# Kernel optimization log

Hardware: AMD Instinct MI355X
Metric: run time of the kernel (lower is better)

## Reference

```python
import jax, jax.numpy as jnp
import numpy as np

B, F_SP, F_DN, VOCAB, EMB = 16384, 26, 13, 100000, 16


def setup_inputs() -> dict:
    key = jax.random.key(0)
    ks = jax.random.split(key, 9)
    sparse_inputs = jax.random.randint(ks[0], (B, F_SP), 0, VOCAB, dtype=jnp.int32)
    dense_inputs = jax.random.normal(ks[1], (B, F_DN), dtype=jnp.float32)
    s = 0.02
    return {
        "sparse_inputs": sparse_inputs,
        "dense_inputs": dense_inputs,
        "linear_dense_W": jax.random.normal(ks[2], (F_DN, 1), jnp.float32) * s,
        "linear_dense_b": jnp.zeros((1,), jnp.float32),
        "linear_emb": jax.random.normal(ks[3], (F_SP, VOCAB, 1), jnp.float32) * s,  # per-feature 1-d linear embeddings
        "fm_emb": jax.random.normal(ks[4], (F_SP, VOCAB, EMB), jnp.float32) * s,    # per-feature FM embeddings
        "finish_W": jax.random.normal(ks[5], (1, 1), jnp.float32) * s,
        "finish_b": jnp.zeros((1,), jnp.float32),
        "like_W": jax.random.normal(ks[6], (1, 1), jnp.float32) * s,
        "like_b": jnp.zeros((1,), jnp.float32),
    }


def reference(sparse_inputs, dense_inputs, linear_dense_W, linear_dense_b,
              linear_emb, fm_emb, finish_W, finish_b, like_W, like_b):
    feat_idx = jnp.arange(F_SP)[None, :]  # [1, F]

    # first-order: dense linear + sum of 1-d sparse embeddings
    lin_dense = dense_inputs @ linear_dense_W + linear_dense_b          # [B, 1]
    lin_sparse = linear_emb[feat_idx, sparse_inputs]                    # [B, F, 1]
    first_order = lin_dense + jnp.sum(lin_sparse, axis=1)               # [B, 1]

    # second-order FM: 0.5 * sum((sum_f v)^2 - sum_f v^2)
    emb = fm_emb[feat_idx, sparse_inputs]                               # [B, F, E]
    summed = jnp.sum(emb, axis=1)                                       # [B, E]
    second_order = 0.5 * jnp.sum(summed * summed - jnp.sum(emb * emb, axis=1),
                                 axis=1, keepdims=True)                 # [B, 1]

    logits = first_order + second_order                                 # [B, 1]
    finish = jax.nn.sigmoid(logits @ finish_W + finish_b)               # [B, 1]
    like = jax.nn.sigmoid(logits @ like_W + like_b)                     # [B, 1]
    return jnp.concatenate([finish, like], axis=1)                      # [B, 2]
```

## Files before the change

kernel.cpp:

```cpp
#include <hip/hip_runtime.h>
#include <math.h>

#define B_TOT 16384
#define F_SP  26
#define F_DN  13
#define VOCAB 100000
#define EMB   16

typedef float fvec2 __attribute__((ext_vector_type(2)));

__global__ __launch_bounds__(256) void fm_mtl_kernel(
    const int*   __restrict__ sparse,
    const float* __restrict__ dense,
    const float* __restrict__ ldW,
    const float* __restrict__ ldB,
    const float* __restrict__ lin_emb,
    const float* __restrict__ fm_emb,
    const float* __restrict__ fW, const float* __restrict__ fB,
    const float* __restrict__ lW, const float* __restrict__ lB,
    float*       __restrict__ out)
{
    __shared__ int s_idx[16 * F_SP];
    const int tid = threadIdx.x;
    const int block_base = blockIdx.x * 16;

    for (int i = tid; i < 16 * F_SP; i += 256)
        s_idx[i] = sparse[block_base * F_SP + i];
    __syncthreads();

    const int sloc = tid >> 4;
    const int g    = tid & 15;
    const int d    = g & 7;
    const int fh   = g >> 3;
    const int b    = block_base + sloc;
    const int* idx = &s_idx[sloc * F_SP];

    float lin = lin_emb[(size_t)g * VOCAB + (size_t)idx[g]];
    if (g < 10)
        lin += lin_emb[(size_t)(g + 16) * VOCAB + (size_t)idx[g + 16]];
    if (g < F_DN)
        lin += dense[b * F_DN + g] * ldW[g];
    if (g == 0)
        lin += ldB[0];

    fvec2 s = (fvec2)(0.f);
    float ssq = 0.f;
    const int f0 = fh * 13;
    #pragma unroll
    for (int k = 0; k < 13; ++k) {
        const int f = f0 + k;
        const int v = idx[f];
        const fvec2* ep = reinterpret_cast<const fvec2*>(
            &fm_emb[((size_t)f * VOCAB + (size_t)v) * EMB + d * 2]);
        const fvec2 e = __builtin_nontemporal_load(ep);
        s += e;
        ssq += e.x * e.x + e.y * e.y;
    }

    s.x += __shfl_xor(s.x, 8);
    s.y += __shfl_xor(s.y, 8);

    const float p2 = s.x * s.x + s.y * s.y;
    float r = 0.25f * p2 - 0.5f * ssq + lin;
    r += __shfl_xor(r, 1);
    r += __shfl_xor(r, 2);
    r += __shfl_xor(r, 4);
    r += __shfl_xor(r, 8);

    if (g == 0) {
        const float finish = 1.f / (1.f + expf(-(r * fW[0] + fB[0])));
        const float like   = 1.f / (1.f + expf(-(r * lW[0] + lB[0])));
        *reinterpret_cast<float2*>(&out[b * 2]) = make_float2(finish, like);
    }
}

extern "C" void kernel_launch(void* const* d_in, const int* in_sizes, int n_in,
                              void* d_out, int out_size, void* d_ws, size_t ws_size,
                              hipStream_t stream) {
    const int*   sparse  = (const int*)  d_in[0];
    const float* dense   = (const float*)d_in[1];
    const float* ldW     = (const float*)d_in[2];
    const float* ldB     = (const float*)d_in[3];
    const float* lin_emb = (const float*)d_in[4];
    const float* fm_emb  = (const float*)d_in[5];
    const float* fW      = (const float*)d_in[6];
    const float* fB      = (const float*)d_in[7];
    const float* lW      = (const float*)d_in[8];
    const float* lB      = (const float*)d_in[9];
    float* out = (float*)d_out;

    fm_mtl_kernel<<<dim3(B_TOT / 16), dim3(256), 0, stream>>>(
        sparse, dense, ldW, ldB, lin_emb, fm_emb, fW, fB, lW, lB, out);
}
```

Before: 20.35 us.

## Use 32 threads per sample and broadcast indices via shuffles instead of LDS

Each sample now gets 32 lanes instead of 16, with features split into four groups of 7/7/6/6. This halves the serial gather chain per lane and doubles the number of outstanding loads. The shared-memory index staging and its barrier are replaced by each lane loading one index and broadcasting it with __shfl. The nontemporal load hint is dropped. The cost is twice as many blocks, an extra shuffle reduction level, and shuffle latency sitting on the dependent gather address path.

```diff
diff --git a/kernel.cpp b/kernel.cpp
--- a/kernel.cpp
+++ b/kernel.cpp
@@ -6,8 +6,6 @@
 #define F_DN  13
 #define VOCAB 100000
 #define EMB   16
-
-typedef float fvec2 __attribute__((ext_vector_type(2)));
 
 __global__ __launch_bounds__(256) void fm_mtl_kernel(
     const int*   __restrict__ sparse,
@@ -20,52 +18,52 @@
     const float* __restrict__ lW, const float* __restrict__ lB,
     float*       __restrict__ out)
 {
-    __shared__ int s_idx[16 * F_SP];
     const int tid = threadIdx.x;
-    const int block_base = blockIdx.x * 16;
+    const int g   = tid & 31;
+    const int b   = blockIdx.x * 8 + (tid >> 5);
+    const int d   = g & 7;
+    const int fq  = g >> 3;
 
-    for (int i = tid; i < 16 * F_SP; i += 256)
-        s_idx[i] = sparse[block_base * F_SP + i];
-    __syncthreads();
-
-    const int sloc = tid >> 4;
-    const int g    = tid & 15;
-    const int d    = g & 7;
-    const int fh   = g >> 3;
-    const int b    = block_base + sloc;
-    const int* idx = &s_idx[sloc * F_SP];
-
-    float lin = lin_emb[(size_t)g * VOCAB + (size_t)idx[g]];
-    if (g < 10)
-        lin += lin_emb[(size_t)(g + 16) * VOCAB + (size_t)idx[g + 16]];
+    int myidx = 0;
+    float lin = 0.f;
+    if (g < F_SP) {
+        myidx = sparse[b * F_SP + g];
+        lin = lin_emb[(size_t)g * VOCAB + (size_t)myidx];
+    }
     if (g < F_DN)
         lin += dense[b * F_DN + g] * ldW[g];
     if (g == 0)
         lin += ldB[0];
 
-    fvec2 s = (fvec2)(0.f);
+    const int f0 = (fq < 2) ? fq * 7 : 14 + (fq - 2) * 6;
+    const int nf = (fq < 2) ? 7 : 6;
+
+    float2 s = make_float2(0.f, 0.f);
     float ssq = 0.f;
-    const int f0 = fh * 13;
     #pragma unroll
-    for (int k = 0; k < 13; ++k) {
-        const int f = f0 + k;
-        const int v = idx[f];
-        const fvec2* ep = reinterpret_cast<const fvec2*>(
-            &fm_emb[((size_t)f * VOCAB + (size_t)v) * EMB + d * 2]);
-        const fvec2 e = __builtin_nontemporal_load(ep);
-        s += e;
-        ssq += e.x * e.x + e.y * e.y;
+    for (int k = 0; k < 7; ++k) {
+        if (k < nf) {
+            const int f = f0 + k;
+            const int v = __shfl(myidx, f, 32);
+            const float2 e = *reinterpret_cast<const float2*>(
+                &fm_emb[((size_t)f * VOCAB + (size_t)v) * EMB + d * 2]);
+            s.x += e.x; s.y += e.y;
+            ssq += e.x * e.x + e.y * e.y;
+        }
     }
 
     s.x += __shfl_xor(s.x, 8);
     s.y += __shfl_xor(s.y, 8);
+    s.x += __shfl_xor(s.x, 16);
+    s.y += __shfl_xor(s.y, 16);
 
     const float p2 = s.x * s.x + s.y * s.y;
-    float r = 0.25f * p2 - 0.5f * ssq + lin;
+    float r = 0.125f * p2 - 0.5f * ssq + lin;
     r += __shfl_xor(r, 1);
     r += __shfl_xor(r, 2);
     r += __shfl_xor(r, 4);
     r += __shfl_xor(r, 8);
+    r += __shfl_xor(r, 16);
 
     if (g == 0) {
         const float finish = 1.f / (1.f + expf(-(r * fW[0] + fB[0])));
@@ -89,6 +87,6 @@
     const float* lB      = (const float*)d_in[9];
     float* out = (float*)d_out;
 
-    fm_mtl_kernel<<<dim3(B_TOT / 16), dim3(256), 0, stream>>>(
+    fm_mtl_kernel<<<dim3(B_TOT / 8), dim3(256), 0, stream>>>(
         sparse, dense, ldW, ldB, lin_emb, fm_emb, fW, fB, lW, lB, out);
 }
```

After: 21.60 us. 6.1% more time.
